# Kernel optimization log

Measured on AMD Instinct MI355X. Metric: run time of the kernel, lower is better.

The kernel has to match this reference:

```python
import jax, jax.numpy as jnp
import numpy as np

L = 28          # num_hidden_layers (kv_cache leading dim = 2*L = 56)
H = 1024        # hidden_size
NH = 8          # num_attention_heads
KVH = 4         # num_key_value_heads
HD = 128        # head_dim
I = 3072        # mlp intermediate size
VC = 4096       # codec vocab size
NCG = 16        # num_code_groups
B = 4
S = 512         # cached seq len
THETA = 1000000.0
EPS = 1e-6


def rmsnorm(x, w):
    v = jnp.mean(jnp.square(x.astype(jnp.float32)), axis=-1, keepdims=True)
    return (x * jax.lax.rsqrt(v + EPS)).astype(x.dtype) * w


def rotate_half(x):
    h = x.shape[-1] // 2
    return jnp.concatenate([-x[..., h:], x[..., :h]], axis=-1)


def setup_inputs() -> dict:
    key = jax.random.key(0)
    ks = jax.random.split(key, 16)
    def f(k, shp, s=0.02):
        return jax.random.normal(k, shp, jnp.float32) * s
    return {
        "cb0_id": jax.random.randint(ks[0], (B, 1), 0, VC),
        "cb1_15_ids": jax.random.randint(ks[1], (B, NCG - 1), 0, VC),
        "trailing_text_embed": f(ks[2], (B, 1, H), 1.0),
        "kv_cache": f(ks[3], (2 * L, B, KVH, S, HD), 1.0),
        "position": jnp.full((B,), S, dtype=jnp.int32),
        "cb0_emb": f(ks[4], (VC, H), 1.0),
        "cp_emb": f(ks[5], (NCG - 1, VC, H), 1.0),
        "Wq": f(ks[6], (L, H, NH * HD)),
        "Wk": f(ks[7], (L, H, KVH * HD)),
        "Wv": f(ks[8], (L, H, KVH * HD)),
        "Wo": f(ks[9], (L, NH * HD, H)),
        "q_norm_w": jnp.ones((L, HD), jnp.float32),
        "k_norm_w": jnp.ones((L, HD), jnp.float32),
        "ln1_w": jnp.ones((L, H), jnp.float32),
        "ln2_w": jnp.ones((L, H), jnp.float32),
        "Wgate": f(ks[10], (L, H, I)),
        "Wup": f(ks[11], (L, H, I)),
        "Wdown": f(ks[12], (L, I, H)),
        "norm_w": jnp.ones((H,), jnp.float32),
        "head_w": f(ks[13], (H, VC)),
    }


def reference(cb0_id, cb1_15_ids, trailing_text_embed, kv_cache, position,
              cb0_emb, cp_emb, Wq, Wk, Wv, Wo, q_norm_w, k_norm_w,
              ln1_w, ln2_w, Wgate, Wup, Wdown, norm_w, head_w):
    n_rep = NH // KVH
    scale = 1.0 / np.sqrt(HD).astype(np.float32)

    # --- codebook embedding sum ---
    e = cb0_emb[cb0_id[:, 0]]                                   # [B,H]
    cp = cp_emb[jnp.arange(NCG - 1)[None, :], cb1_15_ids]       # [B,15,H]
    h = (e + cp.sum(axis=1))[:, None, :] + trailing_text_embed  # [B,1,H]

    # --- rotary at current position; broadcast shape [B,1,1,HD] ---
    inv_freq = 1.0 / (THETA ** (jnp.arange(0, HD, 2, dtype=jnp.float32) / HD))
    freqs = position.astype(jnp.float32)[:, None] * inv_freq[None, :]  # [B,HD/2]
    emb = jnp.concatenate([freqs, freqs], axis=-1)              # [B,HD]
    cos = jnp.cos(emb)[:, None, None, :]
    sin = jnp.sin(emb)[:, None, None, :]

    kv = kv_cache.reshape(L, 2, B, KVH, S, HD)

    def layer(hs, xs):
        wq, wk, wv, wo, qn, kn, l1, l2, wg, wu, wd, kc, vc = xs
        x = rmsnorm(hs, l1)
        q = (x @ wq).reshape(B, 1, NH, HD)
        k = (x @ wk).reshape(B, 1, KVH, HD)
        v = (x @ wv).reshape(B, 1, KVH, HD)
        q = jnp.transpose(rmsnorm(q, qn), (0, 2, 1, 3))   # [B,NH,1,HD]
        k = jnp.transpose(rmsnorm(k, kn), (0, 2, 1, 3))   # [B,KVH,1,HD]
        v = jnp.transpose(v, (0, 2, 1, 3))
        q = q * cos + rotate_half(q) * sin
        k = k * cos + rotate_half(k) * sin
        fk = jnp.concatenate([kc, k], axis=2)             # [B,KVH,S+1,HD]
        fv = jnp.concatenate([vc, v], axis=2)
        # GQA: head h attends kv head h // n_rep == reshape grouping (q_len = 1)
        qg = q.reshape(B, KVH, n_rep, HD)
        scores = jnp.einsum('bgrd,bgsd->bgrs', qg, fk) * scale
        w = jax.nn.softmax(scores.astype(jnp.float32), axis=-1).astype(q.dtype)
        o = jnp.einsum('bgrs,bgsd->bgrd', w, fv).reshape(B, 1, NH * HD)
        hs = hs + o @ wo
        x = rmsnorm(hs, l2)
        hs = hs + (jax.nn.silu(x @ wg) * (x @ wu)) @ wd
        return hs, (k, v)

    xs = (Wq, Wk, Wv, Wo, q_norm_w, k_norm_w, ln1_w, ln2_w,
          Wgate, Wup, Wdown, kv[:, 0], kv[:, 1])
    h, (new_k, new_v) = jax.lax.scan(layer, h, xs)

    h = rmsnorm(h, norm_w)
    past_hidden = h                                       # [B,1,H]
    logits = (h @ head_w)[:, 0, :]                        # [B,VC]

    full_k = jnp.concatenate([kv[:, 0], new_k], axis=3)   # [L,B,KVH,S+1,HD]
    full_v = jnp.concatenate([kv[:, 1], new_v], axis=3)
    new_kv_cache = jnp.stack([full_k, full_v], axis=1).reshape(2 * L, B, KVH, S + 1, HD)
    return logits, new_kv_cache, past_hidden
```

## Files before the change

kernel.cpp:

```cpp
#include <hip/hip_runtime.h>
#include <math.h>

#define L_  28
#define H_  1024
#define NH_ 8
#define KVH_ 4
#define HD_ 128
#define I_  3072
#define VC_ 4096
#define B_  4
#define S_  512
#define EPS_ 1e-6f

#define WS_HA    0
#define WS_HB    4096
#define WS_XFU   8192
#define WS_SSQ1  12288
#define WS_SSQ2  12416
#define WS_SSQF  12544
#define WS_QKVP  12672
#define WS_ATTO  274816
#define WS_ATML  340352
#define WS_OPP   341376
#define WS_GUP   472448
#define WS_DWP   1258880
#define WS_HDP   1455488

__device__ __forceinline__ float wave_reduce_sum(float v) {
    #pragma unroll
    for (int off = 32; off; off >>= 1) v += __shfl_down(v, off);
    return v;
}
__device__ __forceinline__ float wave_reduce_max(float v) {
    #pragma unroll
    for (int off = 32; off; off >>= 1) v = fmaxf(v, __shfl_down(v, off));
    return v;
}

__global__ __launch_bounds__(128) void k_embed(
    const int* __restrict__ cb0, const int* __restrict__ cb1,
    const float* __restrict__ trail, const float* __restrict__ cb0e,
    const float* __restrict__ cpe, float* __restrict__ h)
{
    const int t = threadIdx.x;
    const int b = blockIdx.x >> 3, sl = blockIdx.x & 7;
    const int i = sl * 128 + t;
    float v = cb0e[(size_t)cb0[b] * 1024 + i] + trail[b * 1024 + i];
    #pragma unroll
    for (int j = 0; j < 15; j++)
        v += cpe[((size_t)j * 4096 + cb1[b * 15 + j]) * 1024 + i];
    h[b * 1024 + i] = v;
}

template<int RPW, int NTOT, typename F>
__device__ __forceinline__ void gemv_core(
    const float* __restrict__ W, int ldw, int wcol0, int k0,
    float* __restrict__ xsl, float4* __restrict__ accbuf,
    float* __restrict__ pp, int colblk, int ks, F&& prologue)
{
    const int t = threadIdx.x;
    const int wv = t >> 6, lane = t & 63;
    const float* Wp = W + (size_t)(k0 + wv * RPW) * ldw + wcol0 + lane * 4;
    float4 wreg[RPW];
    #pragma unroll
    for (int i = 0; i < RPW; i++) wreg[i] = *(const float4*)(Wp + (size_t)i * ldw);
    prologue();
    const float4* xs4 = (const float4*)xsl;
    float4 a0 = {0,0,0,0}, a1 = {0,0,0,0}, a2 = {0,0,0,0}, a3 = {0,0,0,0};
    #pragma unroll
    for (int i = 0; i < RPW; i++) {
        float4 w4 = wreg[i];
        float4 xb = xs4[wv * RPW + i];
        a0.x += w4.x * xb.x; a0.y += w4.y * xb.x; a0.z += w4.z * xb.x; a0.w += w4.w * xb.x;
        a1.x += w4.x * xb.y; a1.y += w4.y * xb.y; a1.z += w4.z * xb.y; a1.w += w4.w * xb.y;
        a2.x += w4.x * xb.z; a2.y += w4.y * xb.z; a2.z += w4.z * xb.z; a2.w += w4.w * xb.z;
        a3.x += w4.x * xb.w; a3.y += w4.y * xb.w; a3.z += w4.z * xb.w; a3.w += w4.w * xb.w;
    }
    accbuf[(wv * 64 + lane) * 4 + 0] = a0;
    accbuf[(wv * 64 + lane) * 4 + 1] = a1;
    accbuf[(wv * 64 + lane) * 4 + 2] = a2;
    accbuf[(wv * 64 + lane) * 4 + 3] = a3;
    __syncthreads();
    const int l2 = t >> 2, b2 = t & 3;
    float4 s0 = accbuf[(0 * 64 + l2) * 4 + b2];
    float4 s1 = accbuf[(1 * 64 + l2) * 4 + b2];
    float4 s2 = accbuf[(2 * 64 + l2) * 4 + b2];
    float4 s3 = accbuf[(3 * 64 + l2) * 4 + b2];
    float4 s;
    s.x = s0.x + s1.x + s2.x + s3.x;
    s.y = s0.y + s1.y + s2.y + s3.y;
    s.z = s0.z + s1.z + s2.z + s3.z;
    s.w = s0.w + s1.w + s2.w + s3.w;
    *(float4*)(pp + ((size_t)ks * 4 + b2) * NTOT + colblk * 256 + l2 * 4) = s;
}

template<bool FIRST>
__global__ __launch_bounds__(256) void k_qkv(
    const float* __restrict__ hPrev, const float* __restrict__ dwp,
    const float* __restrict__ ln1,
    const float* __restrict__ Wq, const float* __restrict__ Wk,
    const float* __restrict__ Wv,
    float* __restrict__ hA, float* __restrict__ ssqp1, float* __restrict__ qkvp)
{
    __shared__ float xsl[128];
    __shared__ float4 accbuf[1024];
    __shared__ float sred[128];
    const int t = threadIdx.x;
    const int ks = blockIdx.y, k0 = ks * 32, cb = blockIdx.x;
    const float* W; int ldw, wcol0;
    if (cb < 4)      { W = Wq; ldw = 1024; wcol0 = cb * 256; }
    else if (cb < 6) { W = Wk; ldw = 512;  wcol0 = (cb - 4) * 256; }
    else             { W = Wv; ldw = 512;  wcol0 = (cb - 6) * 256; }
    gemv_core<8, 2048>(W, ldw, wcol0, k0, xsl, accbuf, qkvp, cb, ks, [&]() {
        if (t < 128) {
            const int row = t >> 2, b = t & 3;
            const int gr = k0 + row;
            float hn = hPrev[b * 1024 + gr];
            if (!FIRST) {
                #pragma unroll 16
                for (int c = 0; c < 48; c++) hn += dwp[(size_t)(c * 4 + b) * 1024 + gr];
            }
            sred[t] = hn * hn;
            xsl[row * 4 + b] = hn * ln1[gr];
            if (cb == 0) hA[b * 1024 + gr] = hn;
        }
        __syncthreads();
        if (cb == 0 && t < 4) {
            float s = 0.f;
            #pragma unroll
            for (int r = 0; r < 32; r++) s += sred[r * 4 + t];
            ssqp1[ks * 4 + t] = s;
        }
    });
}

__global__ __launch_bounds__(256) void k_attn(
    const float* __restrict__ qkvp, const float* __restrict__ ssqp1,
    const float* __restrict__ qnw, const float* __restrict__ knw,
    const float* __restrict__ kin, const float* __restrict__ vin,
    float* __restrict__ kout, float* __restrict__ vout,
    const int* __restrict__ pos,
    float* __restrict__ opart, float* __restrict__ mlpart)
{
    __shared__ float Kl[33][129];
    __shared__ float Vl[33][129];
    __shared__ float ql[2][128];
    __shared__ float sc[2][36];
    __shared__ float red[8];
    __shared__ float rms1sh;

    const int t = threadIdx.x;
    const int bg = blockIdx.x, b = bg >> 2, g = bg & 3;
    const int c = blockIdx.y;
    const int lane = t & 63;
    const int r = t >> 7, d = t & 127;
    const float scale = 0.088388347648318447f;

    if (c == 15 && t == 0) {
        float s = 0.f;
        #pragma unroll
        for (int i = 0; i < 32; i++) s += ssqp1[i * 4 + b];
        rms1sh = rsqrtf(s * (1.f / 1024.f) + EPS_);
    }

    const float posf = (float)pos[b];
    const int j = d & 63;
    const float invf = exp2f(-(float)j * 0.31143075889569021f);
    const float ang = posf * invf;
    const float cs = cosf(ang), sn = sinf(ang);
    const int pd = (d < 64) ? d + 64 : d - 64;

    float qraw = 0.f;
    {
        const int n = (2 * g + r) * 128 + d;
        #pragma unroll
        for (int cc = 0; cc < 32; cc++) qraw += qkvp[((size_t)cc * 4 + b) * 2048 + n];
    }
    ql[r][d] = qraw;
    float ssq = wave_reduce_sum(qraw * qraw);
    if (lane == 0) red[t >> 6] = ssq;
    __syncthreads();
    const float rms_q = rsqrtf((red[r * 2] + red[r * 2 + 1]) * (1.f / 128.f) + EPS_);
    float qv = qraw * rms_q * qnw[d];
    float qp = ql[r][pd] * rms_q * qnw[pd];
    float qro = qv * cs + ((d < 64) ? -qp : qp) * sn;

    float kvraw = 0.f;
    if (c == 15) {
        const int base = (t < 128) ? (1024 + g * 128 + d) : (1536 + g * 128 + d);
        #pragma unroll
        for (int cc = 0; cc < 32; cc++) kvraw += qkvp[((size_t)cc * 4 + b) * 2048 + base];
    }
    float kss = wave_reduce_sum((t < 128) ? kvraw * kvraw : 0.f);
    __syncthreads();
    ql[r][d] = qro;
    if (lane == 0 && t < 128) red[t >> 6] = kss;
    if (c == 15) { if (t < 128) Kl[32][d] = kvraw; else Vl[32][d] = kvraw; }
    __syncthreads();
    float newkv = 0.f;
    if (c == 15) {
        if (t < 128) {
            const float rms_k = rsqrtf((red[0] + red[1]) * (1.f / 128.f) + EPS_);
            float kv_ = Kl[32][d] * rms_k * knw[d];
            float kp  = Kl[32][pd] * rms_k * knw[pd];
            newkv = kv_ * cs + ((d < 64) ? -kp : kp) * sn;
        } else {
            newkv = Vl[32][d] * rms1sh;
        }
    }
    __syncthreads();
    const size_t out_bg = (size_t)bg * (513 * 128);
    if (c == 15) {
        if (t < 128) { Kl[32][d] = newkv; kout[out_bg + 512 * 128 + d] = newkv; }
        else         { Vl[32][d] = newkv; vout[out_bg + 512 * 128 + d] = newkv; }
    }

    const size_t in_bg = (size_t)bg * (512 * 128);
    const int s0 = c * 32;
    #pragma unroll
    for (int i = 0; i < 4; i++) {
        int f4 = i * 256 + t;
        int row = f4 >> 5, d0 = (f4 & 31) * 4;
        float4 k4 = *(const float4*)(kin + in_bg + (size_t)(s0 + row) * 128 + d0);
        float4 v4 = *(const float4*)(vin + in_bg + (size_t)(s0 + row) * 128 + d0);
        Kl[row][d0] = k4.x; Kl[row][d0 + 1] = k4.y; Kl[row][d0 + 2] = k4.z; Kl[row][d0 + 3] = k4.w;
        Vl[row][d0] = v4.x; Vl[row][d0 + 1] = v4.y; Vl[row][d0 + 2] = v4.z; Vl[row][d0 + 3] = v4.w;
        *(float4*)(kout + out_bg + (size_t)(s0 + row) * 128 + d0) = k4;
        *(float4*)(vout + out_bg + (size_t)(s0 + row) * 128 + d0) = v4;
    }
    __syncthreads();

    const int nk = (c == 15) ? 33 : 32;
    const int si = d;
    float sv = -1e30f;
    if (si < nk) {
        float a = 0.f;
        #pragma unroll 8
        for (int dd = 0; dd < 128; dd++) a += ql[r][dd] * Kl[si][dd];
        sv = a * scale;
    }
    float mv = wave_reduce_max(sv);
    if (lane == 0) red[t >> 6] = mv;
    __syncthreads();
    const float m = fmaxf(red[r * 2], red[r * 2 + 1]);
    float p = (si < nk) ? expf(sv - m) : 0.f;
    if (si < nk) sc[r][si] = p;
    float lsum = wave_reduce_sum(p);
    __syncthreads();
    if (lane == 0) red[t >> 6] = lsum;
    __syncthreads();
    const float lr = red[r * 2] + red[r * 2 + 1];
    if (d == 0) {
        mlpart[(size_t)((bg * 2 + r) * 16 + c) * 2 + 0] = m;
        mlpart[(size_t)((bg * 2 + r) * 16 + c) * 2 + 1] = lr;
    }
    float o = 0.f;
    for (int s2 = 0; s2 < nk; s2++) o += sc[r][s2] * Vl[s2][d];
    opart[(size_t)((bg * 2 + r) * 16 + c) * 128 + d] = o;
}

__global__ __launch_bounds__(256) void k_oproj(
    const float* __restrict__ atto, const float* __restrict__ atml,
    const float* __restrict__ Wo_l, float* __restrict__ opp)
{
    __shared__ float xsl[128];
    __shared__ float4 accbuf[1024];
    const int t = threadIdx.x;
    const int ks = blockIdx.y, k0 = ks * 32, cb = blockIdx.x;
    gemv_core<8, 1024>(Wo_l, 1024, cb * 256, k0, xsl, accbuf, opp, cb, ks, [&]() {
        if (t < 128) {
            const int kk = t & 31, b = t >> 5;
            const int nrow = k0 + kk;
            const int head = nrow >> 7, dh = nrow & 127;
            const int g = head >> 1, rr = head & 1;
            const size_t base = (size_t)((b * 4 + g) * 2 + rr) * 16;
            float mc[16], lc[16], M = -1e30f;
            #pragma unroll
            for (int cc = 0; cc < 16; cc++) {
                mc[cc] = atml[(base + cc) * 2];
                lc[cc] = atml[(base + cc) * 2 + 1];
                M = fmaxf(M, mc[cc]);
            }
            float Ls = 0.f, o = 0.f;
            #pragma unroll
            for (int cc = 0; cc < 16; cc++) {
                float wch = expf(mc[cc] - M);
                Ls += lc[cc] * wch;
                o += atto[(base + cc) * 128 + dh] * wch;
            }
            xsl[kk * 4 + b] = o / Ls;
        }
        __syncthreads();
    });
}

__global__ __launch_bounds__(256) void k_gateup(
    const float* __restrict__ hA, const float* __restrict__ opp,
    const float* __restrict__ ln2,
    const float* __restrict__ Wg_l, const float* __restrict__ Wu_l,
    float* __restrict__ hB, float* __restrict__ ssqp2, float* __restrict__ gup)
{
    __shared__ float xsl[128];
    __shared__ float4 accbuf[1024];
    __shared__ float sred[128];
    const int t = threadIdx.x;
    const int ks = blockIdx.y, k0 = ks * 32, cb = blockIdx.x;
    const float* W; int wcol0;
    if (cb < 12) { W = Wg_l; wcol0 = cb * 256; }
    else         { W = Wu_l; wcol0 = (cb - 12) * 256; }
    gemv_core<8, 6144>(W, 3072, wcol0, k0, xsl, accbuf, gup, cb, ks, [&]() {
        if (t < 128) {
            const int row = t >> 2, b = t & 3;
            const int gr = k0 + row;
            float hn = hA[b * 1024 + gr];
            #pragma unroll 16
            for (int c = 0; c < 32; c++) hn += opp[(size_t)(c * 4 + b) * 1024 + gr];
            sred[t] = hn * hn;
            xsl[row * 4 + b] = hn * ln2[gr];
            if (cb == 0) hB[b * 1024 + gr] = hn;
        }
        __syncthreads();
        if (cb == 0 && t < 4) {
            float s = 0.f;
            #pragma unroll
            for (int r = 0; r < 32; r++) s += sred[r * 4 + t];
            ssqp2[ks * 4 + t] = s;
        }
    });
}

__global__ __launch_bounds__(256) void k_down(
    const float* __restrict__ gup, const float* __restrict__ ssqp2,
    const float* __restrict__ Wd_l, float* __restrict__ dwp)
{
    __shared__ float xsl[256];
    __shared__ float4 accbuf[1024];
    __shared__ float rmsb[4];
    const int t = threadIdx.x;
    const int ks = blockIdx.y, k0 = ks * 64, cb = blockIdx.x;
    gemv_core<16, 1024>(Wd_l, 1024, cb * 256, k0, xsl, accbuf, dwp, cb, ks, [&]() {
        if (t < 4) {
            float s = 0.f;
            #pragma unroll
            for (int i = 0; i < 32; i++) s += ssqp2[i * 4 + t];
            rmsb[t] = rsqrtf(s * (1.f / 1024.f) + EPS_);
        }
        __syncthreads();
        const int b = t >> 6, kk = t & 63;
        const float rm = rmsb[b];
        float gg = 0.f, uu = 0.f;
        #pragma unroll 8
        for (int cc = 0; cc < 32; cc++) {
            gg += gup[((size_t)cc * 4 + b) * 6144 + k0 + kk];
            uu += gup[((size_t)cc * 4 + b) * 6144 + 3072 + k0 + kk];
        }
        gg *= rm; uu *= rm;
        xsl[kk * 4 + b] = gg / (1.f + expf(-gg)) * uu;
        __syncthreads();
    });
}

__global__ __launch_bounds__(256) void k_head(
    const float* __restrict__ hB, const float* __restrict__ dwp,
    const float* __restrict__ normw, const float* __restrict__ headw,
    float* __restrict__ xfu, float* __restrict__ ssqpF, float* __restrict__ hdp)
{
    __shared__ float xsl[128];
    __shared__ float4 accbuf[1024];
    __shared__ float sred[128];
    const int t = threadIdx.x;
    const int ks = blockIdx.y, k0 = ks * 32, cb = blockIdx.x;
    gemv_core<8, 4096>(headw, 4096, cb * 256, k0, xsl, accbuf, hdp, cb, ks, [&]() {
        if (t < 128) {
            const int row = t >> 2, b = t & 3;
            const int gr = k0 + row;
            float hn = hB[b * 1024 + gr];
            #pragma unroll 16
            for (int c = 0; c < 48; c++) hn += dwp[(size_t)(c * 4 + b) * 1024 + gr];
            sred[t] = hn * hn;
            const float x = hn * normw[gr];
            xsl[row * 4 + b] = x;
            if (cb == 0) xfu[b * 1024 + gr] = x;
        }
        __syncthreads();
        if (cb == 0 && t < 4) {
            float s = 0.f;
            #pragma unroll
            for (int r = 0; r < 32; r++) s += sred[r * 4 + t];
            ssqpF[ks * 4 + t] = s;
        }
    });
}

__global__ __launch_bounds__(256) void k_logits(
    const float* __restrict__ hdp, const float* __restrict__ ssqpF,
    const float* __restrict__ xfu,
    float* __restrict__ logits, float* __restrict__ past)
{
    __shared__ float rsh;
    const int t = threadIdx.x, bid = blockIdx.x;
    const int b = bid >> 2;
    if (t == 0) {
        float s = 0.f;
        #pragma unroll
        for (int i = 0; i < 32; i++) s += ssqpF[i * 4 + b];
        rsh = rsqrtf(s * (1.f / 1024.f) + EPS_);
    }
    __syncthreads();
    const float rf = rsh;
    const int t4 = bid * 256 + t;
    const int n4 = t4 & 1023;
    float4 s = {0.f, 0.f, 0.f, 0.f};
    #pragma unroll
    for (int c = 0; c < 32; c++) {
        float4 v = *(const float4*)(hdp + ((size_t)c * 4 + b) * 4096 + n4 * 4);
        s.x += v.x; s.y += v.y; s.z += v.z; s.w += v.w;
    }
    s.x *= rf; s.y *= rf; s.z *= rf; s.w *= rf;
    *(float4*)(logits + (size_t)t4 * 4) = s;
    if (t < 64) {
        const int p = bid * 64 + t;
        const int i4 = p & 255;
        float4 x = *(const float4*)(xfu + b * 1024 + i4 * 4);
        x.x *= rf; x.y *= rf; x.z *= rf; x.w *= rf;
        *(float4*)(past + (size_t)p * 4) = x;
    }
}

extern "C" void kernel_launch(void* const* d_in, const int* in_sizes, int n_in,
                              void* d_out, int out_size, void* d_ws, size_t ws_size,
                              hipStream_t stream)
{
    const int*   cb0   = (const int*)d_in[0];
    const int*   cb1   = (const int*)d_in[1];
    const float* trail = (const float*)d_in[2];
    const float* kvin  = (const float*)d_in[3];
    const int*   pos   = (const int*)d_in[4];
    const float* cb0e  = (const float*)d_in[5];
    const float* cpe   = (const float*)d_in[6];
    const float* Wq    = (const float*)d_in[7];
    const float* Wk    = (const float*)d_in[8];
    const float* Wv    = (const float*)d_in[9];
    const float* Wo    = (const float*)d_in[10];
    const float* qnw   = (const float*)d_in[11];
    const float* knw   = (const float*)d_in[12];
    const float* ln1   = (const float*)d_in[13];
    const float* ln2   = (const float*)d_in[14];
    const float* Wg    = (const float*)d_in[15];
    const float* Wu    = (const float*)d_in[16];
    const float* Wd    = (const float*)d_in[17];
    const float* normw = (const float*)d_in[18];
    const float* headw = (const float*)d_in[19];

    float* out    = (float*)d_out;
    float* logits = out;
    float* kvout  = out + 16384;
    float* past   = out + 16384 + (size_t)2 * L_ * B_ * KVH_ * (S_ + 1) * HD_;
    float* ws = (float*)d_ws;

    float* hA    = ws + WS_HA;
    float* hB    = ws + WS_HB;
    float* xfu   = ws + WS_XFU;
    float* ssqp1 = ws + WS_SSQ1;
    float* ssqp2 = ws + WS_SSQ2;
    float* ssqpF = ws + WS_SSQF;
    float* qkvp  = ws + WS_QKVP;
    float* atto  = ws + WS_ATTO;
    float* atml  = ws + WS_ATML;
    float* opp   = ws + WS_OPP;
    float* gup   = ws + WS_GUP;
    float* dwp   = ws + WS_DWP;
    float* hdp   = ws + WS_HDP;

    const size_t IN_PLANE  = (size_t)B_ * KVH_ * S_ * HD_;
    const size_t OUT_PLANE = (size_t)B_ * KVH_ * (S_ + 1) * HD_;

    k_embed<<<32, 128, 0, stream>>>(cb0, cb1, trail, cb0e, cpe, hB);

    for (int l = 0; l < L_; l++) {
        if (l == 0)
            k_qkv<true><<<dim3(8, 32), 256, 0, stream>>>(
                hB, dwp, ln1 + (size_t)l * H_,
                Wq + (size_t)l * H_ * 1024, Wk + (size_t)l * H_ * 512,
                Wv + (size_t)l * H_ * 512, hA, ssqp1, qkvp);
        else
            k_qkv<false><<<dim3(8, 32), 256, 0, stream>>>(
                hB, dwp, ln1 + (size_t)l * H_,
                Wq + (size_t)l * H_ * 1024, Wk + (size_t)l * H_ * 512,
                Wv + (size_t)l * H_ * 512, hA, ssqp1, qkvp);
        k_attn<<<dim3(16, 16), 256, 0, stream>>>(
            qkvp, ssqp1, qnw + (size_t)l * HD_, knw + (size_t)l * HD_,
            kvin + (size_t)(2 * l) * IN_PLANE, kvin + (size_t)(2 * l + 1) * IN_PLANE,
            kvout + (size_t)(2 * l) * OUT_PLANE, kvout + (size_t)(2 * l + 1) * OUT_PLANE,
            pos, atto, atml);
        k_oproj<<<dim3(4, 32), 256, 0, stream>>>(
            atto, atml, Wo + (size_t)l * 1024 * H_, opp);
        k_gateup<<<dim3(24, 32), 256, 0, stream>>>(
            hA, opp, ln2 + (size_t)l * H_,
            Wg + (size_t)l * H_ * I_, Wu + (size_t)l * H_ * I_, hB, ssqp2, gup);
        k_down<<<dim3(4, 48), 256, 0, stream>>>(
            gup, ssqp2, Wd + (size_t)l * I_ * H_, dwp);
    }
    k_head<<<dim3(16, 32), 256, 0, stream>>>(hB, dwp, normw, headw, xfu, ssqpF, hdp);
    k_logits<<<16, 256, 0, stream>>>(hdp, ssqpF, xfu, logits, past);
}
```

Baseline: 1.097 ms.

## Fuse embedding into first QKV, use nontemporal loads, double-buffer gate/up weights

Folds the embedding-sum kernel into the first-layer QKV prologue, which removes one launch. Switches weight streaming and KV-cache copy loads and stores to nontemporal builtins so single-use data bypasses the caches. Restructures gate/up so each block handles three column tiles, prefetching the next tile's weights into registers while computing the current one. The block count for that kernel drops from 768 to 256, which trades parallelism for per-block prologue reuse and overlap, and the extra register buffers may reduce occupancy.

```diff
diff --git a/kernel.cpp b/kernel.cpp
--- a/kernel.cpp
+++ b/kernel.cpp
@@ -26,6 +26,17 @@
 #define WS_DWP   1258880
 #define WS_HDP   1455488
 
+typedef float v4f __attribute__((ext_vector_type(4)));
+
+__device__ __forceinline__ float4 ntld4(const float* p) {
+    v4f r = __builtin_nontemporal_load(reinterpret_cast<const v4f*>(p));
+    return make_float4(r.x, r.y, r.z, r.w);
+}
+__device__ __forceinline__ void ntst4(float* p, float4 v) {
+    v4f r = {v.x, v.y, v.z, v.w};
+    __builtin_nontemporal_store(r, reinterpret_cast<v4f*>(p));
+}
+
 __device__ __forceinline__ float wave_reduce_sum(float v) {
     #pragma unroll
     for (int off = 32; off; off >>= 1) v += __shfl_down(v, off);
@@ -35,21 +46,6 @@
     #pragma unroll
     for (int off = 32; off; off >>= 1) v = fmaxf(v, __shfl_down(v, off));
     return v;
-}
-
-__global__ __launch_bounds__(128) void k_embed(
-    const int* __restrict__ cb0, const int* __restrict__ cb1,
-    const float* __restrict__ trail, const float* __restrict__ cb0e,
-    const float* __restrict__ cpe, float* __restrict__ h)
-{
-    const int t = threadIdx.x;
-    const int b = blockIdx.x >> 3, sl = blockIdx.x & 7;
-    const int i = sl * 128 + t;
-    float v = cb0e[(size_t)cb0[b] * 1024 + i] + trail[b * 1024 + i];
-    #pragma unroll
-    for (int j = 0; j < 15; j++)
-        v += cpe[((size_t)j * 4096 + cb1[b * 15 + j]) * 1024 + i];
-    h[b * 1024 + i] = v;
 }
 
 template<int RPW, int NTOT, typename F>
@@ -63,7 +59,7 @@
     const float* Wp = W + (size_t)(k0 + wv * RPW) * ldw + wcol0 + lane * 4;
     float4 wreg[RPW];
     #pragma unroll
-    for (int i = 0; i < RPW; i++) wreg[i] = *(const float4*)(Wp + (size_t)i * ldw);
+    for (int i = 0; i < RPW; i++) wreg[i] = ntld4(Wp + (size_t)i * ldw);
     prologue();
     const float4* xs4 = (const float4*)xsl;
     float4 a0 = {0,0,0,0}, a1 = {0,0,0,0}, a2 = {0,0,0,0}, a3 = {0,0,0,0};
@@ -97,6 +93,9 @@
 template<bool FIRST>
 __global__ __launch_bounds__(256) void k_qkv(
     const float* __restrict__ hPrev, const float* __restrict__ dwp,
+    const int* __restrict__ cb0, const int* __restrict__ cb1,
+    const float* __restrict__ trail, const float* __restrict__ cb0e,
+    const float* __restrict__ cpe,
     const float* __restrict__ ln1,
     const float* __restrict__ Wq, const float* __restrict__ Wk,
     const float* __restrict__ Wv,
@@ -115,8 +114,14 @@
         if (t < 128) {
             const int row = t >> 2, b = t & 3;
             const int gr = k0 + row;
-            float hn = hPrev[b * 1024 + gr];
-            if (!FIRST) {
+            float hn;
+            if (FIRST) {
+                hn = cb0e[(size_t)cb0[b] * 1024 + gr] + trail[b * 1024 + gr];
+                #pragma unroll
+                for (int j = 0; j < 15; j++)
+                    hn += cpe[((size_t)j * 4096 + cb1[b * 15 + j]) * 1024 + gr];
+            } else {
+                hn = hPrev[b * 1024 + gr];
                 #pragma unroll 16
                 for (int c = 0; c < 48; c++) hn += dwp[(size_t)(c * 4 + b) * 1024 + gr];
             }
@@ -221,12 +226,12 @@
     for (int i = 0; i < 4; i++) {
         int f4 = i * 256 + t;
         int row = f4 >> 5, d0 = (f4 & 31) * 4;
-        float4 k4 = *(const float4*)(kin + in_bg + (size_t)(s0 + row) * 128 + d0);
-        float4 v4 = *(const float4*)(vin + in_bg + (size_t)(s0 + row) * 128 + d0);
+        float4 k4 = ntld4(kin + in_bg + (size_t)(s0 + row) * 128 + d0);
+        float4 v4 = ntld4(vin + in_bg + (size_t)(s0 + row) * 128 + d0);
         Kl[row][d0] = k4.x; Kl[row][d0 + 1] = k4.y; Kl[row][d0 + 2] = k4.z; Kl[row][d0 + 3] = k4.w;
         Vl[row][d0] = v4.x; Vl[row][d0 + 1] = v4.y; Vl[row][d0 + 2] = v4.z; Vl[row][d0 + 3] = v4.w;
-        *(float4*)(kout + out_bg + (size_t)(s0 + row) * 128 + d0) = k4;
-        *(float4*)(vout + out_bg + (size_t)(s0 + row) * 128 + d0) = v4;
+        ntst4(kout + out_bg + (size_t)(s0 + row) * 128 + d0, k4);
+        ntst4(vout + out_bg + (size_t)(s0 + row) * 128 + d0, v4);
     }
     __syncthreads();
 
@@ -304,29 +309,78 @@
     __shared__ float4 accbuf[1024];
     __shared__ float sred[128];
     const int t = threadIdx.x;
-    const int ks = blockIdx.y, k0 = ks * 32, cb = blockIdx.x;
-    const float* W; int wcol0;
-    if (cb < 12) { W = Wg_l; wcol0 = cb * 256; }
-    else         { W = Wu_l; wcol0 = (cb - 12) * 256; }
-    gemv_core<8, 6144>(W, 3072, wcol0, k0, xsl, accbuf, gup, cb, ks, [&]() {
-        if (t < 128) {
-            const int row = t >> 2, b = t & 3;
-            const int gr = k0 + row;
-            float hn = hA[b * 1024 + gr];
-            #pragma unroll 16
-            for (int c = 0; c < 32; c++) hn += opp[(size_t)(c * 4 + b) * 1024 + gr];
-            sred[t] = hn * hn;
-            xsl[row * 4 + b] = hn * ln2[gr];
-            if (cb == 0) hB[b * 1024 + gr] = hn;
-        }
-        __syncthreads();
-        if (cb == 0 && t < 4) {
-            float s = 0.f;
+    const int ks = blockIdx.y, k0 = ks * 32, bx = blockIdx.x;
+    const int wv = t >> 6, lane = t & 63;
+    const int u0 = bx * 3;
+
+    float4 wA[8], wB[8];
+    {
+        const float* Wp = ((u0 < 12) ? (Wg_l + u0 * 256) : (Wu_l + (u0 - 12) * 256))
+                          + (size_t)(k0 + wv * 8) * 3072 + lane * 4;
+        #pragma unroll
+        for (int i = 0; i < 8; i++) wA[i] = ntld4(Wp + (size_t)i * 3072);
+    }
+
+    if (t < 128) {
+        const int row = t >> 2, b = t & 3;
+        const int gr = k0 + row;
+        float hn = hA[b * 1024 + gr];
+        #pragma unroll 16
+        for (int c = 0; c < 32; c++) hn += opp[(size_t)(c * 4 + b) * 1024 + gr];
+        sred[t] = hn * hn;
+        xsl[row * 4 + b] = hn * ln2[gr];
+        if (bx == 0) hB[b * 1024 + gr] = hn;
+    }
+    __syncthreads();
+    if (bx == 0 && t < 4) {
+        float s = 0.f;
+        #pragma unroll
+        for (int r = 0; r < 32; r++) s += sred[r * 4 + t];
+        ssqp2[ks * 4 + t] = s;
+    }
+
+    const float4* xs4 = (const float4*)xsl;
+    #pragma unroll
+    for (int j = 0; j < 3; j++) {
+        const int u = u0 + j;
+        if (j < 2) {
+            const int un = u0 + j + 1;
+            const float* Wpn = ((un < 12) ? (Wg_l + un * 256) : (Wu_l + (un - 12) * 256))
+                               + (size_t)(k0 + wv * 8) * 3072 + lane * 4;
+            float4* wn = (j == 0) ? wB : wA;
             #pragma unroll
-            for (int r = 0; r < 32; r++) s += sred[r * 4 + t];
-            ssqp2[ks * 4 + t] = s;
-        }
-    });
+            for (int i = 0; i < 8; i++) wn[i] = ntld4(Wpn + (size_t)i * 3072);
+        }
+        const float4* wc = (j == 1) ? wB : wA;
+        float4 a0 = {0,0,0,0}, a1 = {0,0,0,0}, a2 = {0,0,0,0}, a3 = {0,0,0,0};
+        #pragma unroll
+        for (int i = 0; i < 8; i++) {
+            float4 w4 = wc[i];
+            float4 xb = xs4[wv * 8 + i];
+            a0.x += w4.x * xb.x; a0.y += w4.y * xb.x; a0.z += w4.z * xb.x; a0.w += w4.w * xb.x;
+            a1.x += w4.x * xb.y; a1.y += w4.y * xb.y; a1.z += w4.z * xb.y; a1.w += w4.w * xb.y;
+            a2.x += w4.x * xb.z; a2.y += w4.y * xb.z; a2.z += w4.z * xb.z; a2.w += w4.w * xb.z;
+            a3.x += w4.x * xb.w; a3.y += w4.y * xb.w; a3.z += w4.z * xb.w; a3.w += w4.w * xb.w;
+        }
+        accbuf[(wv * 64 + lane) * 4 + 0] = a0;
+        accbuf[(wv * 64 + lane) * 4 + 1] = a1;
+        accbuf[(wv * 64 + lane) * 4 + 2] = a2;
+        accbuf[(wv * 64 + lane) * 4 + 3] = a3;
+        __syncthreads();
+        const int l2 = t >> 2, b2 = t & 3;
+        float4 s0 = accbuf[(0 * 64 + l2) * 4 + b2];
+        float4 s1 = accbuf[(1 * 64 + l2) * 4 + b2];
+        float4 s2 = accbuf[(2 * 64 + l2) * 4 + b2];
+        float4 s3 = accbuf[(3 * 64 + l2) * 4 + b2];
+        float4 s;
+        s.x = s0.x + s1.x + s2.x + s3.x;
+        s.y = s0.y + s1.y + s2.y + s3.y;
+        s.z = s0.z + s1.z + s2.z + s3.z;
+        s.w = s0.w + s1.w + s2.w + s3.w;
+        const int ucol0 = (u < 12) ? u * 256 : 3072 + (u - 12) * 256;
+        *(float4*)(gup + ((size_t)ks * 4 + b2) * 6144 + ucol0 + l2 * 4) = s;
+        __syncthreads();
+    }
 }
 
 __global__ __launch_bounds__(256) void k_down(
@@ -475,17 +529,15 @@
     const size_t IN_PLANE  = (size_t)B_ * KVH_ * S_ * HD_;
     const size_t OUT_PLANE = (size_t)B_ * KVH_ * (S_ + 1) * HD_;
 
-    k_embed<<<32, 128, 0, stream>>>(cb0, cb1, trail, cb0e, cpe, hB);
-
     for (int l = 0; l < L_; l++) {
         if (l == 0)
             k_qkv<true><<<dim3(8, 32), 256, 0, stream>>>(
-                hB, dwp, ln1 + (size_t)l * H_,
+                hB, dwp, cb0, cb1, trail, cb0e, cpe, ln1 + (size_t)l * H_,
                 Wq + (size_t)l * H_ * 1024, Wk + (size_t)l * H_ * 512,
                 Wv + (size_t)l * H_ * 512, hA, ssqp1, qkvp);
         else
             k_qkv<false><<<dim3(8, 32), 256, 0, stream>>>(
-                hB, dwp, ln1 + (size_t)l * H_,
+                hB, dwp, cb0, cb1, trail, cb0e, cpe, ln1 + (size_t)l * H_,
                 Wq + (size_t)l * H_ * 1024, Wk + (size_t)l * H_ * 512,
                 Wv + (size_t)l * H_ * 512, hA, ssqp1, qkvp);
         k_attn<<<dim3(16, 16), 256, 0, stream>>>(
@@ -495,7 +547,7 @@
             pos, atto, atml);
         k_oproj<<<dim3(4, 32), 256, 0, stream>>>(
             atto, atml, Wo + (size_t)l * 1024 * H_, opp);
-        k_gateup<<<dim3(24, 32), 256, 0, stream>>>(
+        k_gateup<<<dim3(8, 32), 256, 0, stream>>>(
             hA, opp, ln2 + (size_t)l * H_,
             Wg + (size_t)l * H_ * I_, Wu + (size_t)l * H_ * I_, hB, ssqp2, gup);
         k_down<<<dim3(4, 48), 256, 0, stream>>>(
```

Result: no change. 1.093 ms, median of 2 (-0.4%).
